# Kernel tuning notes

Hardware: AMD Instinct MI355X
Metric: run time of the kernel (lower is better)

The kernel has to match this reference:

```python
import jax, jax.numpy as jnp
import numpy as np

T, B, IN, H1, H2, OUT = 1024, 512, 20, 128, 64, 3

def _uniform(key, shape, bound):
    return jax.random.uniform(key, shape, jnp.float32, -bound, bound)

def setup_inputs() -> dict:
    key = jax.random.key(0)
    ks = jax.random.split(key, 11)
    b1 = 1.0 / np.sqrt(H1)
    b2 = 1.0 / np.sqrt(H2)
    return {
        "x": jax.random.normal(ks[0], (T, B, IN), jnp.float32),
        "W_ih0": _uniform(ks[1], (4 * H1, IN), b1),
        "W_hh0": _uniform(ks[2], (4 * H1, H1), b1),
        "b_ih0": _uniform(ks[3], (4 * H1,), b1),
        "b_hh0": _uniform(ks[4], (4 * H1,), b1),
        "W_ih1": _uniform(ks[5], (4 * H2, H1), b2),
        "W_hh1": _uniform(ks[6], (4 * H2, H2), b2),
        "b_ih1": _uniform(ks[7], (4 * H2,), b2),
        "b_hh1": _uniform(ks[8], (4 * H2,), b2),
        "W_d": _uniform(ks[9], (OUT, H2), b2),
        "b_d": _uniform(ks[10], (OUT,), b2),
    }

def _lstm_layer(x, W_ih, W_hh, b_ih, b_hh, hidden):
    # x: (T, B, in_dim); PyTorch gate order: i, f, g, o
    batch = x.shape[1]
    x_proj = jnp.einsum("tbi,gi->tbg", x, W_ih) + (b_ih + b_hh)  # (T,B,4H)

    def step(carry, xp):
        h, c = carry
        gates = xp + h @ W_hh.T  # (B,4H)
        i, f, g, o = jnp.split(gates, 4, axis=-1)
        i = jax.nn.sigmoid(i)
        f = jax.nn.sigmoid(f)
        g = jnp.tanh(g)
        o = jax.nn.sigmoid(o)
        c = f * c + i * g
        h = o * jnp.tanh(c)
        return (h, c), h

    h0 = jnp.zeros((batch, hidden), x.dtype)
    c0 = jnp.zeros((batch, hidden), x.dtype)
    _, ys = jax.lax.scan(step, (h0, c0), x_proj)
    return ys  # (T, B, H)

def reference(x, W_ih0, W_hh0, b_ih0, b_hh0, W_ih1, W_hh1, b_ih1, b_hh1, W_d, b_d):
    h1 = _lstm_layer(x, W_ih0, W_hh0, b_ih0, b_hh0, H1)   # (T,B,128)
    h2 = _lstm_layer(h1, W_ih1, W_hh1, b_ih1, b_hh1, H2)  # (T,B,64)
    # Faithful to original: lstm_out[:, -1, :] in seq-first layout picks the
    # last batch element at every timestep -> (T, 64)
    last = h2[:, -1, :]
    act = jax.nn.relu(last)
    # Dropout in eval mode is identity.
    return act @ W_d.T + b_d  # (T, 3)
```

## Files before the change

### kernel.cpp

```cpp
#include <hip/hip_runtime.h>
#include <hip/hip_bf16.h>


#define T_STEPS 1024
#define BATCH   512
#define IN_F    20
#define H1_     128
#define H2_     64
#define OUT_F   3
#define G1_     (4*H1_)
#define G2_     (4*H2_)

typedef float f4 __attribute__((ext_vector_type(4)));

__device__ __forceinline__ float sigmoidf_(float x) {
    return 1.0f / (1.0f + __expf(-x));
}
__device__ __forceinline__ float tanhf_(float x) {
    return 1.0f - 2.0f / (__expf(2.0f * x) + 1.0f);
}

#define REP8(M)  M(0) M(1) M(2) M(3) M(4) M(5) M(6) M(7)
#define REP16(M) REP8(M) M(8) M(9) M(10) M(11) M(12) M(13) M(14) M(15)

__global__ void xproj_kernel(const float* __restrict__ x,
                             const float* __restrict__ W_ih0,
                             const float* __restrict__ b_ih0,
                             const float* __restrict__ b_hh0,
                             float* __restrict__ xp1)
{
    const int t = blockIdx.x;
    const int g = threadIdx.x;
    const float* xr = x + ((size_t)t * BATCH + (BATCH - 1)) * IN_F;
    const float* w  = W_ih0 + g * IN_F;
    float acc = b_ih0[g] + b_hh0[g];
#pragma unroll
    for (int i = 0; i < IN_F; ++i) acc = fmaf(xr[i], w[i], acc);
    xp1[t * G1_ + g] = acc;
}

__global__ __attribute__((amdgpu_flat_work_group_size(1024, 1024)))
void lstm1_kernel(const float* __restrict__ xp1,
                  const float* __restrict__ W_hh0,
                  float* __restrict__ h1seq)
{
    const int tid = threadIdx.x;
    const int g   = tid & 511;
    const int hf  = tid >> 9;

    __shared__ f4    sh1[H1_ / 4];
    __shared__ float sp1[G1_ * 3];

    const f4* pw = (const f4*)(W_hh0 + (size_t)g * H1_ + hf * 64);
#define DW(k) f4 w_##k = pw[k];
    REP16(DW)
#undef DW
    asm volatile("" : "+v"(w_0), "+v"(w_1), "+v"(w_2), "+v"(w_3),
                      "+v"(w_4), "+v"(w_5), "+v"(w_6), "+v"(w_7),
                      "+v"(w_8), "+v"(w_9), "+v"(w_10), "+v"(w_11),
                      "+v"(w_12), "+v"(w_13), "+v"(w_14), "+v"(w_15));

    if (tid < H1_ / 4) sh1[tid] = f4{0.f, 0.f, 0.f, 0.f};
    float c1 = 0.0f;
    __syncthreads();

    const f4* hb = sh1 + hf * 16;
    float xp_cur = (hf == 0) ? xp1[g] : 0.0f;

    for (int t = 0; t < T_STEPS; ++t) {
        float xp_next = 0.0f;
        {
            const int tn = (t + 1 < T_STEPS) ? (t + 1) : (T_STEPS - 1);
            if (hf == 0) xp_next = xp1[(size_t)tn * G1_ + g];
        }

        float ax = 0.f, ay = 0.f, az = 0.f, aw = 0.f;
#define P1S(k) { const f4 h4 = hb[k];                                        \
        ax = fmaf(w_##k.x, h4.x, ax); ay = fmaf(w_##k.y, h4.y, ay);          \
        az = fmaf(w_##k.z, h4.z, az); aw = fmaf(w_##k.w, h4.w, aw); }
        REP16(P1S)
#undef P1S
        sp1[g * 3 + hf] = ((ax + ay) + (az + aw)) + xp_cur;
        __syncthreads();

        if (tid < H1_) {
            const float vi = sp1[tid * 3]         + sp1[tid * 3 + 1];
            const float vf = sp1[(H1_   + tid)*3] + sp1[(H1_   + tid)*3 + 1];
            const float vg = sp1[(2*H1_ + tid)*3] + sp1[(2*H1_ + tid)*3 + 1];
            const float vo = sp1[(3*H1_ + tid)*3] + sp1[(3*H1_ + tid)*3 + 1];
            c1 = fmaf(sigmoidf_(vf), c1, sigmoidf_(vi) * tanhf_(vg));
            const float h = sigmoidf_(vo) * tanhf_(c1);
            ((float*)sh1)[tid] = h;
            h1seq[(size_t)t * H1_ + tid] = h;
        }
        __syncthreads();
        xp_cur = xp_next;
    }
}

__global__ void xproj2_kernel(const float* __restrict__ h1seq,
                              const float* __restrict__ W_ih1,
                              const float* __restrict__ b_ih1,
                              const float* __restrict__ b_hh1,
                              float* __restrict__ xp2)
{
    const int t = blockIdx.x;
    const int g = threadIdx.x;
    __shared__ f4 sh[H1_ / 4];
    if (g < H1_ / 4) sh[g] = ((const f4*)(h1seq + (size_t)t * H1_))[g];
    __syncthreads();
    const f4* w = (const f4*)(W_ih1 + (size_t)g * H1_);
    float ax = 0.f, ay = 0.f, az = 0.f, aw = 0.f;
#pragma unroll
    for (int k = 0; k < H1_ / 4; ++k) {
        const f4 h4 = sh[k]; const f4 w4 = w[k];
        ax = fmaf(w4.x, h4.x, ax); ay = fmaf(w4.y, h4.y, ay);
        az = fmaf(w4.z, h4.z, az); aw = fmaf(w4.w, h4.w, aw);
    }
    xp2[(size_t)t * G2_ + g] = ((ax + ay) + (az + aw)) + b_ih1[g] + b_hh1[g];
}

__global__ __attribute__((amdgpu_flat_work_group_size(512, 512)))
void lstm2_kernel(const float* __restrict__ xp2,
                  const float* __restrict__ W_hh1,
                  float* __restrict__ h2seq)
{
    const int tid = threadIdx.x;
    const int g   = tid & 255;
    const int hf  = tid >> 8;

    __shared__ f4    sh2[H2_ / 4];
    __shared__ float sp2[G2_ * 3];

    const f4* pw = (const f4*)(W_hh1 + (size_t)g * H2_ + hf * 32);
#define DW(k) f4 w_##k = pw[k];
    REP8(DW)
#undef DW
    asm volatile("" : "+v"(w_0), "+v"(w_1), "+v"(w_2), "+v"(w_3),
                      "+v"(w_4), "+v"(w_5), "+v"(w_6), "+v"(w_7));

    if (tid < H2_ / 4) sh2[tid] = f4{0.f, 0.f, 0.f, 0.f};
    float c2 = 0.0f;
    __syncthreads();

    const f4* hb = sh2 + hf * 8;
    float xp_cur = (hf == 0) ? xp2[g] : 0.0f;

    for (int t = 0; t < T_STEPS; ++t) {
        float xp_next = 0.0f;
        {
            const int tn = (t + 1 < T_STEPS) ? (t + 1) : (T_STEPS - 1);
            if (hf == 0) xp_next = xp2[(size_t)tn * G2_ + g];
        }

        float ax = 0.f, ay = 0.f, az = 0.f, aw = 0.f;
#define P1S(k) { const f4 h4 = hb[k];                                        \
        ax = fmaf(w_##k.x, h4.x, ax); ay = fmaf(w_##k.y, h4.y, ay);          \
        az = fmaf(w_##k.z, h4.z, az); aw = fmaf(w_##k.w, h4.w, aw); }
        REP8(P1S)
#undef P1S
        sp2[g * 3 + hf] = ((ax + ay) + (az + aw)) + xp_cur;
        __syncthreads();

        if (tid < H2_) {
            const float vi = sp2[tid * 3]         + sp2[tid * 3 + 1];
            const float vf = sp2[(H2_   + tid)*3] + sp2[(H2_   + tid)*3 + 1];
            const float vg = sp2[(2*H2_ + tid)*3] + sp2[(2*H2_ + tid)*3 + 1];
            const float vo = sp2[(3*H2_ + tid)*3] + sp2[(3*H2_ + tid)*3 + 1];
            c2 = fmaf(sigmoidf_(vf), c2, sigmoidf_(vi) * tanhf_(vg));
            const float h = sigmoidf_(vo) * tanhf_(c2);
            ((float*)sh2)[tid] = h;
            h2seq[(size_t)t * H2_ + tid] = h;
        }
        __syncthreads();
        xp_cur = xp_next;
    }
}

__global__ void head_kernel(const float* __restrict__ h2seq,
                            const float* __restrict__ W_d,
                            const float* __restrict__ b_d,
                            float* __restrict__ out)
{
    const int idx = blockIdx.x * blockDim.x + threadIdx.x;
    if (idx >= T_STEPS * OUT_F) return;
    const int t = idx / OUT_F;
    const int o = idx - t * OUT_F;
    const float* hr = h2seq + (size_t)t * H2_;
    const float* w  = W_d + o * H2_;
    float acc = b_d[o];
#pragma unroll
    for (int j = 0; j < H2_; ++j) acc = fmaf(fmaxf(hr[j], 0.0f), w[j], acc);
    out[idx] = acc;
}

extern "C" void kernel_launch(void* const* d_in, const int* in_sizes, int n_in,
                              void* d_out, int out_size, void* d_ws, size_t ws_size,
                              hipStream_t stream) {
    const float* x     = (const float*)d_in[0];
    const float* W_ih0 = (const float*)d_in[1];
    const float* W_hh0 = (const float*)d_in[2];
    const float* b_ih0 = (const float*)d_in[3];
    const float* b_hh0 = (const float*)d_in[4];
    const float* W_ih1 = (const float*)d_in[5];
    const float* W_hh1 = (const float*)d_in[6];
    const float* b_ih1 = (const float*)d_in[7];
    const float* b_hh1 = (const float*)d_in[8];
    const float* W_d   = (const float*)d_in[9];
    const float* b_d   = (const float*)d_in[10];

    float* out   = (float*)d_out;
    float* xp1   = (float*)d_ws;
    float* h1seq = xp1 + (size_t)T_STEPS * G1_;
    float* h2seq = h1seq + (size_t)T_STEPS * H1_;
    float* xp2   = xp1;

    hipLaunchKernelGGL(xproj_kernel, dim3(T_STEPS), dim3(G1_), 0, stream,
                       x, W_ih0, b_ih0, b_hh0, xp1);
    hipLaunchKernelGGL(lstm1_kernel, dim3(1), dim3(1024), 0, stream,
                       xp1, W_hh0, h1seq);
    hipLaunchKernelGGL(xproj2_kernel, dim3(T_STEPS), dim3(G2_), 0, stream,
                       h1seq, W_ih1, b_ih1, b_hh1, xp2);
    hipLaunchKernelGGL(lstm2_kernel, dim3(1), dim3(512), 0, stream,
                       xp2, W_hh1, h2seq);
    hipLaunchKernelGGL(head_kernel, dim3((T_STEPS * OUT_F + 255) / 256), dim3(256),
                       0, stream, h2seq, W_d, b_d, out);
}
```

Baseline: 1.590 ms.

## Use one thread per gate in layer-2 LSTM and pin weight loads via asm

The second-layer recurrent kernel drops from 512 to 256 threads. Each thread now owns one full gate row of 64 weights held in registers, which removes the split-K partial-sum pass through shared memory and the extra adds. Weight preloading in both recurrent kernels is now done with explicit inline-asm global loads, and waves-per-EU hints are added. Each layer-2 thread now runs a longer serial dot product per step, traded against fewer waves to synchronize and less shared-memory traffic.

```diff
diff --git a/kernel.cpp b/kernel.cpp
--- a/kernel.cpp
+++ b/kernel.cpp
@@ -20,8 +20,33 @@
     return 1.0f - 2.0f / (__expf(2.0f * x) + 1.0f);
 }
 
-#define REP8(M)  M(0) M(1) M(2) M(3) M(4) M(5) M(6) M(7)
-#define REP16(M) REP8(M) M(8) M(9) M(10) M(11) M(12) M(13) M(14) M(15)
+#define REP16(M) M(0) M(1) M(2) M(3) M(4) M(5) M(6) M(7) \
+                 M(8) M(9) M(10) M(11) M(12) M(13) M(14) M(15)
+
+#define ASM_LOAD_16Q(PTR)                                                     \
+    asm volatile(                                                             \
+        "global_load_dwordx4 %0,  %16, off\n\t"                              \
+        "global_load_dwordx4 %1,  %16, off offset:16\n\t"                    \
+        "global_load_dwordx4 %2,  %16, off offset:32\n\t"                    \
+        "global_load_dwordx4 %3,  %16, off offset:48\n\t"                    \
+        "global_load_dwordx4 %4,  %16, off offset:64\n\t"                    \
+        "global_load_dwordx4 %5,  %16, off offset:80\n\t"                    \
+        "global_load_dwordx4 %6,  %16, off offset:96\n\t"                    \
+        "global_load_dwordx4 %7,  %16, off offset:112\n\t"                   \
+        "global_load_dwordx4 %8,  %16, off offset:128\n\t"                   \
+        "global_load_dwordx4 %9,  %16, off offset:144\n\t"                   \
+        "global_load_dwordx4 %10, %16, off offset:160\n\t"                   \
+        "global_load_dwordx4 %11, %16, off offset:176\n\t"                   \
+        "global_load_dwordx4 %12, %16, off offset:192\n\t"                   \
+        "global_load_dwordx4 %13, %16, off offset:208\n\t"                   \
+        "global_load_dwordx4 %14, %16, off offset:224\n\t"                   \
+        "global_load_dwordx4 %15, %16, off offset:240\n\t"                   \
+        "s_waitcnt vmcnt(0)"                                                  \
+        : "=&v"(w_0), "=&v"(w_1), "=&v"(w_2), "=&v"(w_3),                    \
+          "=&v"(w_4), "=&v"(w_5), "=&v"(w_6), "=&v"(w_7),                    \
+          "=&v"(w_8), "=&v"(w_9), "=&v"(w_10), "=&v"(w_11),                  \
+          "=&v"(w_12), "=&v"(w_13), "=&v"(w_14), "=&v"(w_15)                 \
+        : "v"(PTR))
 
 __global__ void xproj_kernel(const float* __restrict__ x,
                              const float* __restrict__ W_ih0,
@@ -39,7 +64,8 @@
     xp1[t * G1_ + g] = acc;
 }
 
-__global__ __attribute__((amdgpu_flat_work_group_size(1024, 1024)))
+__global__ __attribute__((amdgpu_flat_work_group_size(1024, 1024),
+                          amdgpu_waves_per_eu(4, 4)))
 void lstm1_kernel(const float* __restrict__ xp1,
                   const float* __restrict__ W_hh0,
                   float* __restrict__ h1seq)
@@ -52,13 +78,9 @@
     __shared__ float sp1[G1_ * 3];
 
     const f4* pw = (const f4*)(W_hh0 + (size_t)g * H1_ + hf * 64);
-#define DW(k) f4 w_##k = pw[k];
-    REP16(DW)
-#undef DW
-    asm volatile("" : "+v"(w_0), "+v"(w_1), "+v"(w_2), "+v"(w_3),
-                      "+v"(w_4), "+v"(w_5), "+v"(w_6), "+v"(w_7),
-                      "+v"(w_8), "+v"(w_9), "+v"(w_10), "+v"(w_11),
-                      "+v"(w_12), "+v"(w_13), "+v"(w_14), "+v"(w_15));
+    f4 w_0, w_1, w_2, w_3, w_4, w_5, w_6, w_7,
+       w_8, w_9, w_10, w_11, w_12, w_13, w_14, w_15;
+    ASM_LOAD_16Q(pw);
 
     if (tid < H1_ / 4) sh1[tid] = f4{0.f, 0.f, 0.f, 0.f};
     float c1 = 0.0f;
@@ -120,53 +142,49 @@
     xp2[(size_t)t * G2_ + g] = ((ax + ay) + (az + aw)) + b_ih1[g] + b_hh1[g];
 }
 
-__global__ __attribute__((amdgpu_flat_work_group_size(512, 512)))
+__global__ __attribute__((amdgpu_flat_work_group_size(256, 256),
+                          amdgpu_waves_per_eu(1, 1)))
 void lstm2_kernel(const float* __restrict__ xp2,
                   const float* __restrict__ W_hh1,
                   float* __restrict__ h2seq)
 {
     const int tid = threadIdx.x;
-    const int g   = tid & 255;
-    const int hf  = tid >> 8;
 
     __shared__ f4    sh2[H2_ / 4];
-    __shared__ float sp2[G2_ * 3];
-
-    const f4* pw = (const f4*)(W_hh1 + (size_t)g * H2_ + hf * 32);
-#define DW(k) f4 w_##k = pw[k];
-    REP8(DW)
-#undef DW
-    asm volatile("" : "+v"(w_0), "+v"(w_1), "+v"(w_2), "+v"(w_3),
-                      "+v"(w_4), "+v"(w_5), "+v"(w_6), "+v"(w_7));
+    __shared__ float sg2[G2_];
+
+    const f4* pw = (const f4*)(W_hh1 + (size_t)tid * H2_);
+    f4 w_0, w_1, w_2, w_3, w_4, w_5, w_6, w_7,
+       w_8, w_9, w_10, w_11, w_12, w_13, w_14, w_15;
+    ASM_LOAD_16Q(pw);
 
     if (tid < H2_ / 4) sh2[tid] = f4{0.f, 0.f, 0.f, 0.f};
     float c2 = 0.0f;
     __syncthreads();
 
-    const f4* hb = sh2 + hf * 8;
-    float xp_cur = (hf == 0) ? xp2[g] : 0.0f;
+    float xp_cur = xp2[tid];
 
     for (int t = 0; t < T_STEPS; ++t) {
-        float xp_next = 0.0f;
+        float xp_next;
         {
             const int tn = (t + 1 < T_STEPS) ? (t + 1) : (T_STEPS - 1);
-            if (hf == 0) xp_next = xp2[(size_t)tn * G2_ + g];
+            xp_next = xp2[(size_t)tn * G2_ + tid];
         }
 
         float ax = 0.f, ay = 0.f, az = 0.f, aw = 0.f;
-#define P1S(k) { const f4 h4 = hb[k];                                        \
+#define P1S(k) { const f4 h4 = sh2[k];                                       \
         ax = fmaf(w_##k.x, h4.x, ax); ay = fmaf(w_##k.y, h4.y, ay);          \
         az = fmaf(w_##k.z, h4.z, az); aw = fmaf(w_##k.w, h4.w, aw); }
-        REP8(P1S)
+        REP16(P1S)
 #undef P1S
-        sp2[g * 3 + hf] = ((ax + ay) + (az + aw)) + xp_cur;
+        sg2[tid] = ((ax + ay) + (az + aw)) + xp_cur;
         __syncthreads();
 
         if (tid < H2_) {
-            const float vi = sp2[tid * 3]         + sp2[tid * 3 + 1];
-            const float vf = sp2[(H2_   + tid)*3] + sp2[(H2_   + tid)*3 + 1];
-            const float vg = sp2[(2*H2_ + tid)*3] + sp2[(2*H2_ + tid)*3 + 1];
-            const float vo = sp2[(3*H2_ + tid)*3] + sp2[(3*H2_ + tid)*3 + 1];
+            const float vi = sg2[tid];
+            const float vf = sg2[H2_ + tid];
+            const float vg = sg2[2 * H2_ + tid];
+            const float vo = sg2[3 * H2_ + tid];
             c2 = fmaf(sigmoidf_(vf), c2, sigmoidf_(vi) * tanhf_(vg));
             const float h = sigmoidf_(vo) * tanhf_(c2);
             ((float*)sh2)[tid] = h;
@@ -221,7 +239,7 @@
                        xp1, W_hh0, h1seq);
     hipLaunchKernelGGL(xproj2_kernel, dim3(T_STEPS), dim3(G2_), 0, stream,
                        h1seq, W_ih1, b_ih1, b_hh1, xp2);
-    hipLaunchKernelGGL(lstm2_kernel, dim3(1), dim3(512), 0, stream,
+    hipLaunchKernelGGL(lstm2_kernel, dim3(1), dim3(512 / 2), 0, stream,
                        xp2, W_hh1, h2seq);
     hipLaunchKernelGGL(head_kernel, dim3((T_STEPS * OUT_F + 255) / 256), dim3(256),
                        0, stream, h2seq, W_d, b_d, out);
```

Measured after the change: 1.581 ms. No clear change (-0.6%).

## Pin recurrent weights in AccVGPRs and run gate math uniformly in all threads

Applied to the files above, without the earlier changes.

Moves the per-thread recurrent weight slices of both LSTM layers from ordinary VGPRs into accumulation registers via inline v_accvgpr_write/read, with waves_per_eu hints. This frees architectural registers and avoids spills. The gate nonlinearity block now runs in every thread, using tid&127 or tid&63 as the index, and only the first lanes store h. That removes branch divergence but adds redundant transcendental work and an extra accvgpr read on each weight use inside the serial loop.

```diff
diff --git a/kernel.cpp b/kernel.cpp
--- a/kernel.cpp
+++ b/kernel.cpp
@@ -23,6 +23,21 @@
 #define REP8(M)  M(0) M(1) M(2) M(3) M(4) M(5) M(6) M(7)
 #define REP16(M) REP8(M) M(8) M(9) M(10) M(11) M(12) M(13) M(14) M(15)
 
+#define ADECL(q) float ag##q##_0, ag##q##_1, ag##q##_2, ag##q##_3;
+#define APIN(q, PTR) { const f4 wq_ = (PTR)[q];                               \
+    asm volatile("v_accvgpr_write_b32 %0, %1" : "=a"(ag##q##_0) : "v"(wq_.x));\
+    asm volatile("v_accvgpr_write_b32 %0, %1" : "=a"(ag##q##_1) : "v"(wq_.y));\
+    asm volatile("v_accvgpr_write_b32 %0, %1" : "=a"(ag##q##_2) : "v"(wq_.z));\
+    asm volatile("v_accvgpr_write_b32 %0, %1" : "=a"(ag##q##_3) : "v"(wq_.w));}
+#define AFMA(q, HB)                                                           \
+    { const f4 h4_ = (HB)[q]; float wx_, wy_, wz_, ww_;                       \
+      asm volatile("v_accvgpr_read_b32 %0, %1" : "=v"(wx_) : "a"(ag##q##_0)); \
+      asm volatile("v_accvgpr_read_b32 %0, %1" : "=v"(wy_) : "a"(ag##q##_1)); \
+      asm volatile("v_accvgpr_read_b32 %0, %1" : "=v"(wz_) : "a"(ag##q##_2)); \
+      asm volatile("v_accvgpr_read_b32 %0, %1" : "=v"(ww_) : "a"(ag##q##_3)); \
+      ax = fmaf(wx_, h4_.x, ax); ay = fmaf(wy_, h4_.y, ay);                   \
+      az = fmaf(wz_, h4_.z, az); aw = fmaf(ww_, h4_.w, aw); }
+
 __global__ void xproj_kernel(const float* __restrict__ x,
                              const float* __restrict__ W_ih0,
                              const float* __restrict__ b_ih0,
@@ -39,7 +54,8 @@
     xp1[t * G1_ + g] = acc;
 }
 
-__global__ __attribute__((amdgpu_flat_work_group_size(1024, 1024)))
+__global__ __attribute__((amdgpu_flat_work_group_size(1024, 1024),
+                          amdgpu_waves_per_eu(4, 4)))
 void lstm1_kernel(const float* __restrict__ xp1,
                   const float* __restrict__ W_hh0,
                   float* __restrict__ h1seq)
@@ -47,18 +63,16 @@
     const int tid = threadIdx.x;
     const int g   = tid & 511;
     const int hf  = tid >> 9;
+    const int hi  = tid & 127;
 
     __shared__ f4    sh1[H1_ / 4];
     __shared__ float sp1[G1_ * 3];
 
     const f4* pw = (const f4*)(W_hh0 + (size_t)g * H1_ + hf * 64);
-#define DW(k) f4 w_##k = pw[k];
-    REP16(DW)
-#undef DW
-    asm volatile("" : "+v"(w_0), "+v"(w_1), "+v"(w_2), "+v"(w_3),
-                      "+v"(w_4), "+v"(w_5), "+v"(w_6), "+v"(w_7),
-                      "+v"(w_8), "+v"(w_9), "+v"(w_10), "+v"(w_11),
-                      "+v"(w_12), "+v"(w_13), "+v"(w_14), "+v"(w_15));
+    REP16(ADECL)
+#define APIN1(q) APIN(q, pw)
+    REP16(APIN1)
+#undef APIN1
 
     if (tid < H1_ / 4) sh1[tid] = f4{0.f, 0.f, 0.f, 0.f};
     float c1 = 0.0f;
@@ -75,23 +89,23 @@
         }
 
         float ax = 0.f, ay = 0.f, az = 0.f, aw = 0.f;
-#define P1S(k) { const f4 h4 = hb[k];                                        \
-        ax = fmaf(w_##k.x, h4.x, ax); ay = fmaf(w_##k.y, h4.y, ay);          \
-        az = fmaf(w_##k.z, h4.z, az); aw = fmaf(w_##k.w, h4.w, aw); }
+#define P1S(k) AFMA(k, hb)
         REP16(P1S)
 #undef P1S
         sp1[g * 3 + hf] = ((ax + ay) + (az + aw)) + xp_cur;
         __syncthreads();
 
-        if (tid < H1_) {
-            const float vi = sp1[tid * 3]         + sp1[tid * 3 + 1];
-            const float vf = sp1[(H1_   + tid)*3] + sp1[(H1_   + tid)*3 + 1];
-            const float vg = sp1[(2*H1_ + tid)*3] + sp1[(2*H1_ + tid)*3 + 1];
-            const float vo = sp1[(3*H1_ + tid)*3] + sp1[(3*H1_ + tid)*3 + 1];
+        {
+            const float vi = sp1[hi * 3]            + sp1[hi * 3 + 1];
+            const float vf = sp1[(H1_   + hi) * 3]  + sp1[(H1_   + hi) * 3 + 1];
+            const float vg = sp1[(2*H1_ + hi) * 3]  + sp1[(2*H1_ + hi) * 3 + 1];
+            const float vo = sp1[(3*H1_ + hi) * 3]  + sp1[(3*H1_ + hi) * 3 + 1];
             c1 = fmaf(sigmoidf_(vf), c1, sigmoidf_(vi) * tanhf_(vg));
             const float h = sigmoidf_(vo) * tanhf_(c1);
-            ((float*)sh1)[tid] = h;
-            h1seq[(size_t)t * H1_ + tid] = h;
+            if (tid < H1_) {
+                ((float*)sh1)[tid] = h;
+                h1seq[(size_t)t * H1_ + tid] = h;
+            }
         }
         __syncthreads();
         xp_cur = xp_next;
@@ -120,57 +134,58 @@
     xp2[(size_t)t * G2_ + g] = ((ax + ay) + (az + aw)) + b_ih1[g] + b_hh1[g];
 }
 
-__global__ __attribute__((amdgpu_flat_work_group_size(512, 512)))
+__global__ __attribute__((amdgpu_flat_work_group_size(512, 512),
+                          amdgpu_waves_per_eu(2, 2)))
 void lstm2_kernel(const float* __restrict__ xp2,
                   const float* __restrict__ W_hh1,
                   float* __restrict__ h2seq)
 {
     const int tid = threadIdx.x;
-    const int g   = tid & 255;
+    const int g2  = tid & 255;
     const int hf  = tid >> 8;
+    const int hi  = tid & 63;
 
     __shared__ f4    sh2[H2_ / 4];
     __shared__ float sp2[G2_ * 3];
 
-    const f4* pw = (const f4*)(W_hh1 + (size_t)g * H2_ + hf * 32);
-#define DW(k) f4 w_##k = pw[k];
-    REP8(DW)
-#undef DW
-    asm volatile("" : "+v"(w_0), "+v"(w_1), "+v"(w_2), "+v"(w_3),
-                      "+v"(w_4), "+v"(w_5), "+v"(w_6), "+v"(w_7));
+    const f4* pw = (const f4*)(W_hh1 + (size_t)g2 * H2_ + hf * 32);
+    REP8(ADECL)
+#define APIN2(q) APIN(q, pw)
+    REP8(APIN2)
+#undef APIN2
 
     if (tid < H2_ / 4) sh2[tid] = f4{0.f, 0.f, 0.f, 0.f};
     float c2 = 0.0f;
     __syncthreads();
 
     const f4* hb = sh2 + hf * 8;
-    float xp_cur = (hf == 0) ? xp2[g] : 0.0f;
+    float xp_cur = (hf == 0) ? xp2[g2] : 0.0f;
 
     for (int t = 0; t < T_STEPS; ++t) {
         float xp_next = 0.0f;
         {
             const int tn = (t + 1 < T_STEPS) ? (t + 1) : (T_STEPS - 1);
-            if (hf == 0) xp_next = xp2[(size_t)tn * G2_ + g];
+            if (hf == 0) xp_next = xp2[(size_t)tn * G2_ + g2];
         }
 
         float ax = 0.f, ay = 0.f, az = 0.f, aw = 0.f;
-#define P1S(k) { const f4 h4 = hb[k];                                        \
-        ax = fmaf(w_##k.x, h4.x, ax); ay = fmaf(w_##k.y, h4.y, ay);          \
-        az = fmaf(w_##k.z, h4.z, az); aw = fmaf(w_##k.w, h4.w, aw); }
-        REP8(P1S)
-#undef P1S
-        sp2[g * 3 + hf] = ((ax + ay) + (az + aw)) + xp_cur;
-        __syncthreads();
-
-        if (tid < H2_) {
-            const float vi = sp2[tid * 3]         + sp2[tid * 3 + 1];
-            const float vf = sp2[(H2_   + tid)*3] + sp2[(H2_   + tid)*3 + 1];
-            const float vg = sp2[(2*H2_ + tid)*3] + sp2[(2*H2_ + tid)*3 + 1];
-            const float vo = sp2[(3*H2_ + tid)*3] + sp2[(3*H2_ + tid)*3 + 1];
+#define P2S(k) AFMA(k, hb)
+        REP8(P2S)
+#undef P2S
+        sp2[g2 * 3 + hf] = ((ax + ay) + (az + aw)) + xp_cur;
+        __syncthreads();
+
+        {
+            const float vi = sp2[hi * 3]           + sp2[hi * 3 + 1];
+            const float vf = sp2[(H2_   + hi) * 3] + sp2[(H2_   + hi) * 3 + 1];
+            const float vg = sp2[(2*H2_ + hi) * 3] + sp2[(2*H2_ + hi) * 3 + 1];
+            const float vo = sp2[(3*H2_ + hi) * 3] + sp2[(3*H2_ + hi) * 3 + 1];
             c2 = fmaf(sigmoidf_(vf), c2, sigmoidf_(vi) * tanhf_(vg));
             const float h = sigmoidf_(vo) * tanhf_(c2);
-            ((float*)sh2)[tid] = h;
-            h2seq[(size_t)t * H2_ + tid] = h;
+            if (tid < H2_) {
+                ((float*)sh2)[tid] = h;
+                h2seq[(size_t)t * H2_ + tid] = h;
+            }
         }
         __syncthreads();
         xp_cur = xp_next;
```

New measurement: 2.164 ms. 1.36x slower.
